# Optimization experiments

Hardware: AMD Instinct MI355X
Metric: run time of the kernel (lower is better)

## Reference

```python
import math
import jax, jax.numpy as jnp
import numpy as np

N_HEAD = 16

def _rope_sin_cos(pos, head_dim, base=10000.0):
    # matches build_sin_cos(seq_len, dim=head_dim//2): inv = base^(-2i/head_dim)
    inv = jnp.exp(jnp.arange(0, head_dim, 2, dtype=jnp.float32) * (-math.log(base) / head_dim))  # (Dh//2,)
    ang = pos[:, None].astype(jnp.float32) * inv[None, :]  # (T, Dh//2)
    return jnp.sin(ang), jnp.cos(ang)

def _apply_rope(q, k, sin, cos):
    # q, k: (B, T, H, Dh); sin/cos: (T, Dh//2)
    half = q.shape[-1] // 2
    s = sin[None, :, None, :]
    c = cos[None, :, None, :]
    q1, q2 = q[..., :half], q[..., half:]
    k1, k2 = k[..., :half], k[..., half:]
    q_rot = jnp.concatenate([q1 * c - q2 * s, q2 * c + q1 * s], axis=-1)
    k_rot = jnp.concatenate([k1 * c - k2 * s, k2 * c + k1 * s], axis=-1)
    return q_rot, k_rot

def setup_inputs() -> dict:
    key = jax.random.key(0)
    k0, k1, k2 = jax.random.split(key, 3)
    B, T, D = 2, 2048, 2048
    x = jax.random.normal(k0, (B, T, D), dtype=jnp.float32)
    w_qkv = jax.random.normal(k1, (3 * D, D), dtype=jnp.float32) * (D ** -0.5)
    w_proj = jax.random.normal(k2, (D, D), dtype=jnp.float32) * (D ** -0.5)
    return {"x": x, "w_qkv": w_qkv, "w_proj": w_proj, "seq_offset": 0}

def reference(x, w_qkv, w_proj, seq_offset):
    # Single-device (world_size=1) ring attention: one hop, so the online
    # lse-merge is the identity; exact causal flash attention + RoPE.
    B, T, D = x.shape
    H = N_HEAD
    Dh = D // H
    qkv = (x @ w_qkv.T).reshape(B, T, 3, H, Dh)
    q, k, v = qkv[:, :, 0], qkv[:, :, 1], qkv[:, :, 2]  # (B, T, H, Dh)
    pos = seq_offset + jnp.arange(T)
    sin, cos = _rope_sin_cos(pos, Dh)
    q, k = _apply_rope(q, k, sin, cos)
    scale = 1.0 / math.sqrt(Dh)  # flash-attn default softmax_scale
    scores = jnp.einsum('bthd,bshd->bhts', q, k) * scale  # (B, H, T, T)
    causal = jnp.tril(jnp.ones((T, T), dtype=bool))
    scores = jnp.where(causal[None, None], scores, -jnp.inf)
    attn = jax.nn.softmax(scores, axis=-1)
    ctx = jnp.einsum('bhts,bshd->bthd', attn, v)  # (B, T, H, Dh)
    out = ctx.reshape(B, T, D) @ w_proj.T
    return out
```

## Files before the change

kernel.cpp:

```cpp
#include <hip/hip_runtime.h>
#include <math.h>

typedef __bf16 bf16x8 __attribute__((ext_vector_type(8)));
typedef float f32x4 __attribute__((ext_vector_type(4)));
typedef unsigned short u16;
typedef unsigned short u16x4 __attribute__((ext_vector_type(4)));
typedef unsigned short u16x8 __attribute__((ext_vector_type(8)));
typedef unsigned int u32;

#define AS1 __attribute__((address_space(1)))
#define AS3 __attribute__((address_space(3)))

static __device__ __forceinline__ float bf2f(u16 u) {
  union { u32 i; float f; } v; v.i = ((u32)u) << 16; return v.f;
}
static __device__ __forceinline__ u16 f2bf(float f) {
  union { __bf16 b; u16 u; } v; v.b = (__bf16)f; return v.u;
}

__global__ __launch_bounds__(256)
void conv_all(const float* __restrict__ x, const float* __restrict__ wq,
              const float* __restrict__ wp, u16* __restrict__ dst) {
  const int gid = blockIdx.x * 256 + threadIdx.x;
  const float* src;
  int off;
  if (gid < 2097152) { src = x; off = gid; }
  else if (gid < 2097152 + 3145728) { src = wq; off = gid - 2097152; }
  else { src = wp; off = gid - (2097152 + 3145728); }
  const float4 v = ((const float4*)src)[off];
  u16x4 p = {f2bf(v.x), f2bf(v.y), f2bf(v.z), f2bf(v.w)};
  ((u16x4*)dst)[gid] = p;
}

template <bool CF32>
__global__ __launch_bounds__(256, 4)
void gemm_bt(const u16* __restrict__ A, const u16* __restrict__ B,
             void* __restrict__ Cp, int M, int N, int K) {
  __shared__ __align__(16) u16 As[128 * 32];
  __shared__ __align__(16) u16 Bs[128 * 32];
  const int tid = threadIdx.x;
  const int lane = tid & 63;
  const int wid = tid >> 6;
  const int wr = wid >> 1, wc = wid & 1;
  const int l15 = lane & 15, l4 = lane >> 4;
  const int m0 = blockIdx.y * 128, n0 = blockIdx.x * 128;

  const f32x4 fzero = {0.f, 0.f, 0.f, 0.f};
  f32x4 acc[4][4];
#pragma unroll
  for (int i = 0; i < 4; ++i)
#pragma unroll
    for (int j = 0; j < 4; ++j) acc[i][j] = fzero;

  for (int kt = 0; kt < K; kt += 32) {
#pragma unroll
    for (int i = 0; i < 2; ++i) {
      const int c = wid * 64 + i * 256 + lane;
      const u16* ga = A + (size_t)(m0 + (c >> 2)) * K + kt + (c & 3) * 8;
      const u16* gb = B + (size_t)(n0 + (c >> 2)) * K + kt + (c & 3) * 8;
      __builtin_amdgcn_global_load_lds((AS1 void*)ga,
          (AS3 void*)(As + (size_t)(wid * 64 + i * 256) * 8), 16, 0, 0);
      __builtin_amdgcn_global_load_lds((AS1 void*)gb,
          (AS3 void*)(Bs + (size_t)(wid * 64 + i * 256) * 8), 16, 0, 0);
    }
    __syncthreads();
    bf16x8 af[4], bfr[4];
#pragma unroll
    for (int m = 0; m < 4; ++m)
      af[m] = *(const bf16x8*)&As[(wr * 64 + m * 16 + l15) * 32 + l4 * 8];
#pragma unroll
    for (int n = 0; n < 4; ++n)
      bfr[n] = *(const bf16x8*)&Bs[(wc * 64 + n * 16 + l15) * 32 + l4 * 8];
#pragma unroll
    for (int m = 0; m < 4; ++m)
#pragma unroll
      for (int n = 0; n < 4; ++n)
        acc[m][n] = __builtin_amdgcn_mfma_f32_16x16x32_bf16(af[m], bfr[n], acc[m][n], 0, 0, 0);
    __syncthreads();
  }

#pragma unroll
  for (int m = 0; m < 4; ++m)
#pragma unroll
    for (int r = 0; r < 4; ++r) {
      const int gm = m0 + wr * 64 + m * 16 + l4 * 4 + r;
      if constexpr (CF32) {
        float* crow = (float*)Cp + (size_t)gm * N + n0 + wc * 64 + l15;
#pragma unroll
        for (int n = 0; n < 4; ++n) crow[n * 16] = acc[m][n][r];
      } else {
        u16* crow = (u16*)Cp + (size_t)gm * N + n0 + wc * 64 + l15;
#pragma unroll
        for (int n = 0; n < 4; ++n) crow[n * 16] = f2bf(acc[m][n][r]);
      }
    }
}

__global__ __launch_bounds__(256)
void rope_kernel(u16* __restrict__ qkv, const int* __restrict__ seq_off) {
  const int idx = blockIdx.x * 256 + threadIdx.x;
  const int d8 = idx & 7;
  const int h = (idx >> 3) & 15;
  const int t = (idx >> 7) & 2047;
  const int b = idx >> 18;
  const int d0 = d8 * 8;
  const float pos = (float)(seq_off[0] + t);
  const size_t base = ((size_t)(b * 2048 + t)) * 6144 + h * 128 + d0;
  const u16x8 qlo = *(const u16x8*)(qkv + base);
  const u16x8 qhi = *(const u16x8*)(qkv + base + 64);
  const u16x8 klo = *(const u16x8*)(qkv + base + 2048);
  const u16x8 khi = *(const u16x8*)(qkv + base + 2048 + 64);
  u16x8 qlo_o, qhi_o, klo_o, khi_o;
#pragma unroll
  for (int j = 0; j < 8; ++j) {
    const float inv = expf((float)(d0 + j) * (-0.14391156509731588f));
    float sv, cv;
    sincosf(pos * inv, &sv, &cv);
    const float q1 = bf2f(qlo[j]), q2 = bf2f(qhi[j]);
    qlo_o[j] = f2bf(q1 * cv - q2 * sv);
    qhi_o[j] = f2bf(q2 * cv + q1 * sv);
    const float k1 = bf2f(klo[j]), k2 = bf2f(khi[j]);
    klo_o[j] = f2bf(k1 * cv - k2 * sv);
    khi_o[j] = f2bf(k2 * cv + k1 * sv);
  }
  *(u16x8*)(qkv + base) = qlo_o;
  *(u16x8*)(qkv + base + 64) = qhi_o;
  *(u16x8*)(qkv + base + 2048) = klo_o;
  *(u16x8*)(qkv + base + 2048 + 64) = khi_o;
}

__global__ __launch_bounds__(256, 2)
void attn_kernel(const u16* __restrict__ qkv, u16* __restrict__ ctx) {
  __shared__ __align__(16) u16 kbuf[2][2][32 * 128];
  __shared__ __align__(16) u16 vbuf[2][2][128 * 32];
  __shared__ __align__(16) u16 Plds[4][2][16 * 32];
  const int tid = threadIdx.x, lane = tid & 63, w = tid >> 6;
  const int l15 = lane & 15, l4 = lane >> 4;
  const int bh = blockIdx.y;
  const int b = bh >> 4, h = bh & 15;
  const u16* Qb = qkv + (size_t)b * 2048 * 6144 + h * 128;
  const u16* Kb = Qb + 2048;
  const u16* Vb = Qb + 4096;

  const int sp = tid & 15;
  const int sB = tid >> 4;
  const int sgp = sB & 1;
  const int swg = (((sp >> 2) ^ (sB & 3)) << 3) + ((sp & 3) << 1);
  const int ks0 = (w * 2 + 0) * 64 + lane;
  const int ks1 = (w * 2 + 1) * 64 + lane;
  const int kr0 = ks0 >> 4, kc0 = (ks0 & 15) ^ (kr0 & 15);
  const int kr1 = ks1 >> 4, kc1 = (ks1 & 15) ^ (kr1 & 15);

  const float scale = 0.08838834764831845f;
  const float M0 = 12.0f;
  const f32x4 fzero = {0.f, 0.f, 0.f, 0.f};

  for (int pass = 0; pass < 2; ++pass) {
    const int qt = pass ? (int)blockIdx.x : (31 - (int)blockIdx.x);
    const int q0 = qt * 64 + w * 16;
    const int nt64 = qt + 1;

    bf16x8 qf[4];
#pragma unroll
    for (int c = 0; c < 4; ++c)
      qf[c] = *(const bf16x8*)(Qb + (size_t)(q0 + l15) * 6144 + c * 32 + l4 * 8);

    f32x4 o[8];
#pragma unroll
    for (int ch = 0; ch < 8; ++ch) o[ch] = fzero;
    float lpart[4] = {0.f, 0.f, 0.f, 0.f};

    __syncthreads();
#pragma unroll
    for (int hh = 0; hh < 2; ++hh) {
      __builtin_amdgcn_global_load_lds(
          (AS1 void*)(Kb + (size_t)(hh * 32 + kr0) * 6144 + kc0 * 8),
          (AS3 void*)(&kbuf[0][hh][(w * 2 + 0) * 512]), 16, 0, 0);
      __builtin_amdgcn_global_load_lds(
          (AS1 void*)(Kb + (size_t)(hh * 32 + kr1) * 6144 + kc1 * 8),
          (AS3 void*)(&kbuf[0][hh][(w * 2 + 1) * 512]), 16, 0, 0);
      const u16* vp = Vb + (size_t)(hh * 32 + 2 * sp) * 6144 + 8 * sB;
      const u16x8 v0 = *(const u16x8*)vp;
      const u16x8 v1 = *(const u16x8*)(vp + 6144);
#pragma unroll
      for (int e = 0; e < 8; ++e) {
        const int s = e ^ sgp;
        const int dh = 8 * sB + s;
        *(u32*)&vbuf[0][hh][dh * 32 + swg] = (u32)v0[s] | ((u32)v1[s] << 16);
      }
    }
    __syncthreads();

    for (int t = 0; t < nt64; ++t) {
      const int cur = t & 1, nxtb = cur ^ 1;
      const int kv0 = t * 64;
      const bool has_next = (t + 1 < nt64);
      u16x8 va0, va1, vb0, vb1;
      if (has_next) {
        const u16* vp = Vb + (size_t)(kv0 + 64 + 2 * sp) * 6144 + 8 * sB;
        va0 = *(const u16x8*)vp;
        va1 = *(const u16x8*)(vp + 6144);
        const u16* vp2 = vp + (size_t)32 * 6144;
        vb0 = *(const u16x8*)vp2;
        vb1 = *(const u16x8*)(vp2 + 6144);
      }
      f32x4 sv[4];
      sv[0] = fzero; sv[1] = fzero; sv[2] = fzero; sv[3] = fzero;
#pragma unroll
      for (int hh = 0; hh < 2; ++hh) {
#pragma unroll
        for (int c = 0; c < 4; ++c) {
          const bf16x8 kf = *(const bf16x8*)&kbuf[cur][hh][l15 * 128 + (((c * 4 + l4) ^ l15) << 3)];
          sv[hh * 2] = __builtin_amdgcn_mfma_f32_16x16x32_bf16(qf[c], kf, sv[hh * 2], 0, 0, 0);
        }
#pragma unroll
        for (int c = 0; c < 4; ++c) {
          const bf16x8 kf = *(const bf16x8*)&kbuf[cur][hh][(16 + l15) * 128 + (((c * 4 + l4) ^ l15) << 3)];
          sv[hh * 2 + 1] = __builtin_amdgcn_mfma_f32_16x16x32_bf16(qf[c], kf, sv[hh * 2 + 1], 0, 0, 0);
        }
      }
      if (has_next) {
#pragma unroll
        for (int hh = 0; hh < 2; ++hh) {
          __builtin_amdgcn_global_load_lds(
              (AS1 void*)(Kb + (size_t)(kv0 + 64 + hh * 32 + kr0) * 6144 + kc0 * 8),
              (AS3 void*)(&kbuf[nxtb][hh][(w * 2 + 0) * 512]), 16, 0, 0);
          __builtin_amdgcn_global_load_lds(
              (AS1 void*)(Kb + (size_t)(kv0 + 64 + hh * 32 + kr1) * 6144 + kc1 * 8),
              (AS3 void*)(&kbuf[nxtb][hh][(w * 2 + 1) * 512]), 16, 0, 0);
        }
      }
#pragma unroll
      for (int hh = 0; hh < 2; ++hh) {
        const int kb0 = kv0 + hh * 32;
        if (kb0 + 31 <= q0) {
#pragma unroll
          for (int r = 0; r < 4; ++r) {
            const float p0 = __expf(fmaf(sv[hh * 2][r], scale, -M0));
            const float p1 = __expf(fmaf(sv[hh * 2 + 1][r], scale, -M0));
            lpart[r] += p0 + p1;
            const int row = l4 * 4 + r;
            const int g0 = ((l15 >> 3) ^ l4) & 3;
            const int g1 = (((l15 >> 3) | 2) ^ l4) & 3;
            Plds[w][hh][row * 32 + g0 * 8 + (l15 & 7)] = f2bf(p0);
            Plds[w][hh][row * 32 + g1 * 8 + (l15 & 7)] = f2bf(p1);
          }
        } else {
#pragma unroll
          for (int r = 0; r < 4; ++r) {
            const int qg = q0 + l4 * 4 + r;
            const float p0 = (kb0 + l15 <= qg) ? __expf(fmaf(sv[hh * 2][r], scale, -M0)) : 0.f;
            const float p1 = (kb0 + 16 + l15 <= qg) ? __expf(fmaf(sv[hh * 2 + 1][r], scale, -M0)) : 0.f;
            lpart[r] += p0 + p1;
            const int row = l4 * 4 + r;
            const int g0 = ((l15 >> 3) ^ l4) & 3;
            const int g1 = (((l15 >> 3) | 2) ^ l4) & 3;
            Plds[w][hh][row * 32 + g0 * 8 + (l15 & 7)] = f2bf(p0);
            Plds[w][hh][row * 32 + g1 * 8 + (l15 & 7)] = f2bf(p1);
          }
        }
      }
      __syncthreads();
      const bf16x8 pa0 = *(const bf16x8*)&Plds[w][0][l15 * 32 + ((l4 ^ (l15 >> 2)) << 3)];
      const bf16x8 pa1 = *(const bf16x8*)&Plds[w][1][l15 * 32 + ((l4 ^ (l15 >> 2)) << 3)];
#pragma unroll
      for (int ch = 0; ch < 8; ++ch) {
        const int dh = ch * 16 + l15;
        const int g = (l4 ^ ((2 * ch + (l15 >> 3)) & 3)) << 3;
        const bf16x8 vf0 = *(const bf16x8*)&vbuf[cur][0][dh * 32 + g];
        o[ch] = __builtin_amdgcn_mfma_f32_16x16x32_bf16(pa0, vf0, o[ch], 0, 0, 0);
        const bf16x8 vf1 = *(const bf16x8*)&vbuf[cur][1][dh * 32 + g];
        o[ch] = __builtin_amdgcn_mfma_f32_16x16x32_bf16(pa1, vf1, o[ch], 0, 0, 0);
      }
      if (has_next) {
#pragma unroll
        for (int e = 0; e < 8; ++e) {
          const int s = e ^ sgp;
          const int dh = 8 * sB + s;
          *(u32*)&vbuf[nxtb][0][dh * 32 + swg] = (u32)va0[s] | ((u32)va1[s] << 16);
          *(u32*)&vbuf[nxtb][1][dh * 32 + swg] = (u32)vb0[s] | ((u32)vb1[s] << 16);
        }
      }
    }
    float invl[4];
#pragma unroll
    for (int r = 0; r < 4; ++r) {
      float l = lpart[r];
      l += __shfl_xor(l, 1);
      l += __shfl_xor(l, 2);
      l += __shfl_xor(l, 4);
      l += __shfl_xor(l, 8);
      invl[r] = 1.0f / l;
    }
#pragma unroll
    for (int ch = 0; ch < 8; ++ch)
#pragma unroll
      for (int r = 0; r < 4; ++r) {
        const int gq = q0 + l4 * 4 + r;
        ctx[(size_t)(b * 2048 + gq) * 2048 + h * 128 + ch * 16 + l15] =
            f2bf(o[ch][r] * invl[r]);
      }
  }
}

extern "C" void kernel_launch(void* const* d_in, const int* in_sizes, int n_in,
                              void* d_out, int out_size, void* d_ws, size_t ws_size,
                              hipStream_t stream) {
  const float* x     = (const float*)d_in[0];
  const float* wqkv  = (const float*)d_in[1];
  const float* wproj = (const float*)d_in[2];
  const int*   soff  = (const int*)d_in[3];
  float* out = (float*)d_out;

  u16* wsu    = (u16*)d_ws;
  u16* xb     = wsu;
  u16* wqkvb  = xb + 8388608;
  u16* wprojb = wqkvb + 12582912;
  u16* qkv    = wprojb + 4194304;
  u16* ctx    = xb;

  conv_all<<<24576, 256, 0, stream>>>(x, wqkv, wproj, wsu);

  gemm_bt<false><<<dim3(48, 32), 256, 0, stream>>>(xb, wqkvb, qkv, 4096, 6144, 2048);
  rope_kernel<<<2048, 256, 0, stream>>>(qkv, soff);
  attn_kernel<<<dim3(16, 32), 256, 0, stream>>>(qkv, ctx);
  gemm_bt<true><<<dim3(16, 32), 256, 0, stream>>>(ctx, wprojb, out, 4096, 2048, 2048);
}
```

Baseline: 299.1 us.

## Double GEMM K-tile with XOR-swizzled LDS and fuse Q RoPE into attention

```diff
diff --git a/kernel.cpp b/kernel.cpp
--- a/kernel.cpp
+++ b/kernel.cpp
@@ -36,8 +36,8 @@
 __global__ __launch_bounds__(256, 4)
 void gemm_bt(const u16* __restrict__ A, const u16* __restrict__ B,
              void* __restrict__ Cp, int M, int N, int K) {
-  __shared__ __align__(16) u16 As[128 * 32];
-  __shared__ __align__(16) u16 Bs[128 * 32];
+  __shared__ __align__(16) u16 As[128 * 64];
+  __shared__ __align__(16) u16 Bs[128 * 64];
   const int tid = threadIdx.x;
   const int lane = tid & 63;
   const int wid = tid >> 6;
@@ -45,6 +45,14 @@
   const int l15 = lane & 15, l4 = lane >> 4;
   const int m0 = blockIdx.y * 128, n0 = blockIdx.x * 128;
 
+  int grow[4], gkc[4];
+#pragma unroll
+  for (int i = 0; i < 4; ++i) {
+    const int idx = i * 256 + tid;
+    grow[i] = idx >> 3;
+    gkc[i] = ((idx & 7) ^ (grow[i] & 7)) * 8;
+  }
+
   const f32x4 fzero = {0.f, 0.f, 0.f, 0.f};
   f32x4 acc[4][4];
 #pragma unroll
@@ -52,30 +60,39 @@
 #pragma unroll
     for (int j = 0; j < 4; ++j) acc[i][j] = fzero;
 
-  for (int kt = 0; kt < K; kt += 32) {
-#pragma unroll
-    for (int i = 0; i < 2; ++i) {
-      const int c = wid * 64 + i * 256 + lane;
-      const u16* ga = A + (size_t)(m0 + (c >> 2)) * K + kt + (c & 3) * 8;
-      const u16* gb = B + (size_t)(n0 + (c >> 2)) * K + kt + (c & 3) * 8;
-      __builtin_amdgcn_global_load_lds((AS1 void*)ga,
-          (AS3 void*)(As + (size_t)(wid * 64 + i * 256) * 8), 16, 0, 0);
-      __builtin_amdgcn_global_load_lds((AS1 void*)gb,
-          (AS3 void*)(Bs + (size_t)(wid * 64 + i * 256) * 8), 16, 0, 0);
+  for (int kt = 0; kt < K; kt += 64) {
+#pragma unroll
+    for (int i = 0; i < 4; ++i) {
+      __builtin_amdgcn_global_load_lds(
+          (AS1 void*)(A + (size_t)(m0 + grow[i]) * K + kt + gkc[i]),
+          (AS3 void*)(As + (size_t)(i * 256 + tid) * 8), 16, 0, 0);
+      __builtin_amdgcn_global_load_lds(
+          (AS1 void*)(B + (size_t)(n0 + grow[i]) * K + kt + gkc[i]),
+          (AS3 void*)(Bs + (size_t)(i * 256 + tid) * 8), 16, 0, 0);
     }
     __syncthreads();
-    bf16x8 af[4], bfr[4];
+    bf16x8 af[4][2], bfr[4][2];
+#pragma unroll
+    for (int m = 0; m < 4; ++m) {
+      const int ra = wr * 64 + m * 16 + l15;
+#pragma unroll
+      for (int ks = 0; ks < 2; ++ks)
+        af[m][ks] = *(const bf16x8*)&As[ra * 64 + (((ks * 4 + l4) ^ (ra & 7)) << 3)];
+    }
+#pragma unroll
+    for (int n = 0; n < 4; ++n) {
+      const int rb = wc * 64 + n * 16 + l15;
+#pragma unroll
+      for (int ks = 0; ks < 2; ++ks)
+        bfr[n][ks] = *(const bf16x8*)&Bs[rb * 64 + (((ks * 4 + l4) ^ (rb & 7)) << 3)];
+    }
 #pragma unroll
     for (int m = 0; m < 4; ++m)
-      af[m] = *(const bf16x8*)&As[(wr * 64 + m * 16 + l15) * 32 + l4 * 8];
-#pragma unroll
-    for (int n = 0; n < 4; ++n)
-      bfr[n] = *(const bf16x8*)&Bs[(wc * 64 + n * 16 + l15) * 32 + l4 * 8];
-#pragma unroll
-    for (int m = 0; m < 4; ++m)
-#pragma unroll
-      for (int n = 0; n < 4; ++n)
-        acc[m][n] = __builtin_amdgcn_mfma_f32_16x16x32_bf16(af[m], bfr[n], acc[m][n], 0, 0, 0);
+#pragma unroll
+      for (int n = 0; n < 4; ++n) {
+        acc[m][n] = __builtin_amdgcn_mfma_f32_16x16x32_bf16(af[m][0], bfr[n][0], acc[m][n], 0, 0, 0);
+        acc[m][n] = __builtin_amdgcn_mfma_f32_16x16x32_bf16(af[m][1], bfr[n][1], acc[m][n], 0, 0, 0);
+      }
     __syncthreads();
   }
 
@@ -97,7 +114,7 @@
 }
 
 __global__ __launch_bounds__(256)
-void rope_kernel(u16* __restrict__ qkv, const int* __restrict__ seq_off) {
+void rope_k(u16* __restrict__ qkv, const int* __restrict__ seq_off) {
   const int idx = blockIdx.x * 256 + threadIdx.x;
   const int d8 = idx & 7;
   const int h = (idx >> 3) & 15;
@@ -105,32 +122,26 @@
   const int b = idx >> 18;
   const int d0 = d8 * 8;
   const float pos = (float)(seq_off[0] + t);
-  const size_t base = ((size_t)(b * 2048 + t)) * 6144 + h * 128 + d0;
-  const u16x8 qlo = *(const u16x8*)(qkv + base);
-  const u16x8 qhi = *(const u16x8*)(qkv + base + 64);
-  const u16x8 klo = *(const u16x8*)(qkv + base + 2048);
-  const u16x8 khi = *(const u16x8*)(qkv + base + 2048 + 64);
-  u16x8 qlo_o, qhi_o, klo_o, khi_o;
+  const size_t base = ((size_t)(b * 2048 + t)) * 6144 + h * 128 + d0 + 2048;
+  const u16x8 klo = *(const u16x8*)(qkv + base);
+  const u16x8 khi = *(const u16x8*)(qkv + base + 64);
+  u16x8 klo_o, khi_o;
 #pragma unroll
   for (int j = 0; j < 8; ++j) {
     const float inv = expf((float)(d0 + j) * (-0.14391156509731588f));
     float sv, cv;
     sincosf(pos * inv, &sv, &cv);
-    const float q1 = bf2f(qlo[j]), q2 = bf2f(qhi[j]);
-    qlo_o[j] = f2bf(q1 * cv - q2 * sv);
-    qhi_o[j] = f2bf(q2 * cv + q1 * sv);
     const float k1 = bf2f(klo[j]), k2 = bf2f(khi[j]);
     klo_o[j] = f2bf(k1 * cv - k2 * sv);
     khi_o[j] = f2bf(k2 * cv + k1 * sv);
   }
-  *(u16x8*)(qkv + base) = qlo_o;
-  *(u16x8*)(qkv + base + 64) = qhi_o;
-  *(u16x8*)(qkv + base + 2048) = klo_o;
-  *(u16x8*)(qkv + base + 2048 + 64) = khi_o;
+  *(u16x8*)(qkv + base) = klo_o;
+  *(u16x8*)(qkv + base + 64) = khi_o;
 }
 
 __global__ __launch_bounds__(256, 2)
-void attn_kernel(const u16* __restrict__ qkv, u16* __restrict__ ctx) {
+void attn_kernel(const u16* __restrict__ qkv, u16* __restrict__ ctx,
+                 const int* __restrict__ seq_off) {
   __shared__ __align__(16) u16 kbuf[2][2][32 * 128];
   __shared__ __align__(16) u16 vbuf[2][2][128 * 32];
   __shared__ __align__(16) u16 Plds[4][2][16 * 32];
@@ -154,6 +165,7 @@
   const float scale = 0.08838834764831845f;
   const float M0 = 12.0f;
   const f32x4 fzero = {0.f, 0.f, 0.f, 0.f};
+  const int so = seq_off[0];
 
   for (int pass = 0; pass < 2; ++pass) {
     const int qt = pass ? (int)blockIdx.x : (31 - (int)blockIdx.x);
@@ -164,6 +176,21 @@
 #pragma unroll
     for (int c = 0; c < 4; ++c)
       qf[c] = *(const bf16x8*)(Qb + (size_t)(q0 + l15) * 6144 + c * 32 + l4 * 8);
+    {
+      const float pos = (float)(so + q0 + l15);
+#pragma unroll
+      for (int c = 0; c < 2; ++c)
+#pragma unroll
+        for (int j = 0; j < 8; ++j) {
+          const int d = c * 32 + l4 * 8 + j;
+          const float inv = expf((float)d * (-0.14391156509731588f));
+          float sv, cv;
+          sincosf(pos * inv, &sv, &cv);
+          const float a = (float)qf[c][j], bb = (float)qf[c + 2][j];
+          qf[c][j] = (__bf16)(a * cv - bb * sv);
+          qf[c + 2][j] = (__bf16)(bb * cv + a * sv);
+        }
+    }
 
     f32x4 o[8];
 #pragma unroll
@@ -322,7 +349,7 @@
   conv_all<<<24576, 256, 0, stream>>>(x, wqkv, wproj, wsu);
 
   gemm_bt<false><<<dim3(48, 32), 256, 0, stream>>>(xb, wqkvb, qkv, 4096, 6144, 2048);
-  rope_kernel<<<2048, 256, 0, stream>>>(qkv, soff);
-  attn_kernel<<<dim3(16, 32), 256, 0, stream>>>(qkv, ctx);
+  rope_k<<<2048, 256, 0, stream>>>(qkv, soff);
+  attn_kernel<<<dim3(16, 32), 256, 0, stream>>>(qkv, ctx, soff);
   gemm_bt<true><<<dim3(16, 32), 256, 0, stream>>>(ctx, wprojb, out, 4096, 2048, 2048);
 }
```

Measured after the change: 260.8 us. 1.15x faster.
